# Performance work log

Hardware: AMD Instinct MI355X
Metric: run time of the kernel (lower is better)

Reference implementation:

```python
import math
import jax, jax.numpy as jnp
import numpy as np

NUM_HEADS = 8
FACTOR = 5


def setup_inputs() -> dict:
    key = jax.random.key(0)
    ks = jax.random.split(key, 8)
    B, N, C = 8, 4096, 512
    s = 0.02
    x = jax.random.normal(ks[0], (B, N, C), dtype=jnp.float32)
    Wq = jax.random.normal(ks[1], (C, C), dtype=jnp.float32) * s
    Wk = jax.random.normal(ks[2], (C, C), dtype=jnp.float32) * s
    Wv = jax.random.normal(ks[3], (C, C), dtype=jnp.float32) * s
    Wp = jax.random.normal(ks[4], (C, C), dtype=jnp.float32) * s
    bq = jnp.zeros((C,), jnp.float32)
    bk = jnp.zeros((C,), jnp.float32)
    bv = jnp.zeros((C,), jnp.float32)
    bp = jnp.zeros((C,), jnp.float32)
    sample_k = min(FACTOR * int(np.ceil(np.log(N))), N)  # 45
    index_sample = jax.random.randint(ks[5], (N, sample_k), 0, N, dtype=jnp.int64)
    return {"x": x, "Wq": Wq, "bq": bq, "Wk": Wk, "bk": bk,
            "Wv": Wv, "bv": bv, "Wp": Wp, "bp": bp,
            "index_sample": index_sample}


def reference(x, Wq, bq, Wk, bk, Wv, bv, Wp, bp, index_sample):
    B, N, C = x.shape
    H = NUM_HEADS
    Dh = C // H
    L_Q = L_K = N
    # qkv projections (torch Linear: x @ W.T + b; W sampled symmetric so use x @ W + b)
    q = (x @ Wq + bq).reshape(B, N, H, Dh).transpose(0, 2, 1, 3)  # [B,H,L,Dh]
    k = (x @ Wk + bk).reshape(B, N, H, Dh).transpose(0, 2, 1, 3)
    v = (x @ Wv + bv).reshape(B, N, H, Dh).transpose(0, 2, 1, 3)

    u = min(FACTOR * int(np.ceil(np.log(L_Q))), L_Q)  # n_top
    scale = (C // H) ** (-0.5)

    # _prob_QK: sampled scores per query
    K_sample = k[:, :, index_sample, :]                       # [B,H,L_Q,s,Dh]
    QK_sample = jnp.einsum('bhld,bhlsd->bhls', q, K_sample)   # [B,H,L_Q,s]
    M = QK_sample.max(axis=-1) - QK_sample.sum(axis=-1) / L_K # sparsity measure
    _, M_top = jax.lax.top_k(M, u)                            # [B,H,u]
    Q_reduce = jnp.take_along_axis(q, M_top[..., None], axis=2)  # [B,H,u,Dh]
    scores = jnp.einsum('bhud,bhkd->bhuk', Q_reduce, k) * scale  # [B,H,u,L_K]

    # initial context: mean of V over keys (mask_flag=False)
    context = jnp.broadcast_to(v.mean(axis=2, keepdims=True), (B, H, L_Q, Dh))

    # update context at selected queries
    attn = jax.nn.softmax(scores, axis=-1)
    out_u = jnp.einsum('bhuk,bhkd->bhud', attn, v)            # [B,H,u,Dh]
    bI = jnp.arange(B)[:, None, None]
    hI = jnp.arange(H)[None, :, None]
    context = context.at[bI, hI, M_top].set(out_u)            # [B,H,L_Q,Dh]

    # mix=True: reshape [B,H,N,Dh] -> [B,N,H*Dh] directly (faithful to source)
    context = context.reshape(B, N, H * Dh)
    return context @ Wp + bp
```

## Files before the change

### kernel.cpp

```cpp
#include <hip/hip_runtime.h>
#include <float.h>

typedef unsigned short ushort_t;
typedef short bf16x8 __attribute__((ext_vector_type(8)));
typedef _Float16 f16x8 __attribute__((ext_vector_type(8)));
typedef float f32x4 __attribute__((ext_vector_type(4)));

#define NS 4096
#define ND 64
#define NU 45
#define NUP 48

__device__ __forceinline__ float bf2f(ushort_t u){ return __uint_as_float(((unsigned)u)<<16); }
__device__ __forceinline__ ushort_t f2bf(float f){
  unsigned u = __float_as_uint(f);
  u += 0x7fffu + ((u>>16)&1u);
  return (ushort_t)(u>>16);
}
__device__ __forceinline__ ushort_t f2h(float f){ _Float16 h=(_Float16)f; return __builtin_bit_cast(ushort_t, h); }
__device__ __forceinline__ float h2f(ushort_t u){ return (float)__builtin_bit_cast(_Float16, u); }

__global__ __launch_bounds__(256) void k_wsplit(const float* __restrict__ Wq,
                                                const float* __restrict__ Wk,
                                                const float* __restrict__ Wv,
                                                ushort_t* __restrict__ wh,
                                                ushort_t* __restrict__ wl)
{
  int i = blockIdx.x*256 + threadIdx.x;
  int c = i >> 9, k = i & 511;
  const float* W = (c < 512) ? Wq : (c < 1024 ? Wk : Wv);
  float v = W[k*512 + (c & 511)];
  ushort_t h = f2bf(v);
  wh[i] = h;
  wl[i] = f2bf(v - bf2f(h));
}

__global__ __launch_bounds__(256) void k_xsplit(const float* __restrict__ x,
                                                ushort_t* __restrict__ xh,
                                                ushort_t* __restrict__ xl)
{
  int i = (blockIdx.x*256 + threadIdx.x)*4;
  float4 v = *(const float4*)(x + i);
  ushort4 h, lo;
  h.x = f2bf(v.x); lo.x = f2bf(v.x - bf2f(h.x));
  h.y = f2bf(v.y); lo.y = f2bf(v.y - bf2f(h.y));
  h.z = f2bf(v.z); lo.z = f2bf(v.z - bf2f(h.z));
  h.w = f2bf(v.w); lo.w = f2bf(v.w - bf2f(h.w));
  *(ushort4*)(xh + i) = h;
  *(ushort4*)(xl + i) = lo;
}

template<int MODE>
__global__ __launch_bounds__(256) void k_gemm(
    const float* __restrict__ x,
    const ushort_t* __restrict__ xh, const ushort_t* __restrict__ xl,
    const ushort_t* __restrict__ wh, const ushort_t* __restrict__ wl,
    const float* __restrict__ bq, const float* __restrict__ bk, const float* __restrict__ bv,
    float* __restrict__ qf, float* __restrict__ kf, ushort_t* __restrict__ vfT,
    ushort_t* __restrict__ kb16)
{
  __shared__ __align__(16) ushort_t smem[20480];
  ushort_t* Ah = smem;
  ushort_t* Al = smem + 5120;
  ushort_t* Bh = smem + 10240;
  ushort_t* Bl = smem + 15360;
  const int nbx = (MODE == 0) ? 4 : 8;
  const int p = blockIdx.y * nbx + blockIdx.x;
  const int cx = p & 7;
  const int local = p >> 3;
  const int by = cx*32 + local/nbx;
  const int bx = local % nbx;
  const int rowbase = by * 128;
  const int colbase = (MODE == 0 ? 0 : 512) + bx*128;
  const int mat = colbase >> 9;
  const int t = threadIdx.x;
  const int l = t & 63;
  const int w = t >> 6;
  const int wm = w >> 1, wn = w & 1;
  f32x4 acc[4][4] = {};
  const int r0 = t >> 2;
  const int c0 = (t & 3) * 8;

  for (int k0 = 0; k0 < 512; k0 += 32) {
    __syncthreads();
    #pragma unroll
    for (int half = 0; half < 2; half++) {
      const int r = r0 + half*64;
      if constexpr (MODE == 1) {
        *(uint4*)(&Ah[r*40 + c0]) = *(const uint4*)(&xh[(size_t)(rowbase + r)*512 + k0 + c0]);
        *(uint4*)(&Al[r*40 + c0]) = *(const uint4*)(&xl[(size_t)(rowbase + r)*512 + k0 + c0]);
      } else {
        const float* xp = &x[(size_t)(rowbase + r)*512 + k0 + c0];
        float4 v0 = *(const float4*)xp;
        float4 v1 = *(const float4*)(xp + 4);
        ushort_t hi[8], lo[8];
        float vv[8] = {v0.x,v0.y,v0.z,v0.w,v1.x,v1.y,v1.z,v1.w};
        #pragma unroll
        for (int j = 0; j < 8; j++) {
          hi[j] = f2bf(vv[j]);
          lo[j] = f2bf(vv[j] - bf2f(hi[j]));
        }
        *(uint4*)(&Ah[r*40 + c0]) = *(const uint4*)hi;
        *(uint4*)(&Al[r*40 + c0]) = *(const uint4*)lo;
      }
      *(uint4*)(&Bh[r*40 + c0]) = *(const uint4*)(&wh[(size_t)(colbase + r)*512 + k0 + c0]);
      *(uint4*)(&Bl[r*40 + c0]) = *(const uint4*)(&wl[(size_t)(colbase + r)*512 + k0 + c0]);
    }
    __syncthreads();
    bf16x8 ah[4], al[4], bh8[4], bl8[4];
    #pragma unroll
    for (int m = 0; m < 4; m++) {
      const int off = (wm*64 + m*16 + (l & 15))*40 + (l >> 4)*8;
      ah[m] = *(const bf16x8*)(&Ah[off]);
      al[m] = *(const bf16x8*)(&Al[off]);
    }
    #pragma unroll
    for (int n = 0; n < 4; n++) {
      const int off = (wn*64 + n*16 + (l & 15))*40 + (l >> 4)*8;
      bh8[n] = *(const bf16x8*)(&Bh[off]);
      bl8[n] = *(const bf16x8*)(&Bl[off]);
    }
    #pragma unroll
    for (int m = 0; m < 4; m++)
      #pragma unroll
      for (int n = 0; n < 4; n++) {
        acc[m][n] = __builtin_amdgcn_mfma_f32_16x16x32_bf16(ah[m], bh8[n], acc[m][n], 0, 0, 0);
        acc[m][n] = __builtin_amdgcn_mfma_f32_16x16x32_bf16(ah[m], bl8[n], acc[m][n], 0, 0, 0);
        acc[m][n] = __builtin_amdgcn_mfma_f32_16x16x32_bf16(al[m], bh8[n], acc[m][n], 0, 0, 0);
      }
  }

  if (MODE == 0 || mat == 1) {
    const float* bias_p = (MODE == 0) ? bq : bk;
    float* dst = (MODE == 0) ? qf : kf;
    #pragma unroll
    for (int n = 0; n < 4; n++) {
      const int wi = (colbase & 511) + wn*64 + n*16 + (l & 15);
      const int hh = wi >> 6, d = wi & 63;
      const float bias = bias_p[wi];
      #pragma unroll
      for (int m = 0; m < 4; m++) {
        const int rb = rowbase + wm*64 + m*16 + ((l >> 4) << 2);
        const int b  = rb >> 12, nr = rb & 4095;
        #pragma unroll
        for (int j = 0; j < 4; j++)
          dst[((size_t)(b*8 + hh)*NS + nr + j)*ND + d] = acc[m][n][j] + bias;
      }
    }
    if (MODE == 1 && kb16) {
      __syncthreads();
      #pragma unroll
      for (int n = 0; n < 4; n++) {
        const int c_l = wn*64 + n*16 + (l & 15);
        const float bias = bk[(colbase & 511) + c_l];
        #pragma unroll
        for (int m = 0; m < 4; m++) {
          const int rb_l = wm*64 + m*16 + ((l >> 4) << 2);
          #pragma unroll
          for (int j = 0; j < 4; j++)
            smem[(rb_l + j)*136 + c_l] = f2bf(acc[m][n][j] + bias);
        }
      }
      __syncthreads();
      const int r2 = t >> 1, half = t & 1;
      const int hh2 = ((colbase & 511) >> 6) + half;
      const int b2 = rowbase >> 12;
      const int nr2 = rowbase & 4095;
      ushort_t* op = &kb16[((size_t)(b2*8 + hh2)*NS + nr2 + r2)*ND];
      const ushort_t* ip = &smem[r2*136 + half*64];
      #pragma unroll
      for (int cch = 0; cch < 8; cch++)
        *(uint4*)(op + cch*8) = *(const uint4*)(ip + cch*8);
    }
  } else {
    __syncthreads();
    #pragma unroll
    for (int n = 0; n < 4; n++) {
      const int wi_l = wn*64 + n*16 + (l & 15);
      const float bias = bv[(colbase & 511) + wi_l];
      #pragma unroll
      for (int m = 0; m < 4; m++) {
        const int nr_l = wm*64 + m*16 + ((l >> 4) << 2);
        ushort4 pk;
        pk.x = f2h(acc[m][n][0] + bias);
        pk.y = f2h(acc[m][n][1] + bias);
        pk.z = f2h(acc[m][n][2] + bias);
        pk.w = f2h(acc[m][n][3] + bias);
        *(ushort4*)(&smem[wi_l*136 + nr_l]) = pk;
      }
    }
    __syncthreads();
    const int wi2 = t >> 1, half = t & 1;
    const int cim = (colbase & 511) + wi2;
    const int hh2 = cim >> 6, d2 = cim & 63;
    const int b2 = rowbase >> 12;
    const int nr2 = (rowbase & 4095) + half*64;
    ushort_t* op = &vfT[((size_t)(b2*8 + hh2)*ND + d2)*NS + nr2];
    const ushort_t* ip = &smem[wi2*136 + half*64];
    #pragma unroll
    for (int cch = 0; cch < 8; cch++)
      *(uint4*)(op + cch*8) = *(const uint4*)(ip + cch*8);
  }
}

__global__ __launch_bounds__(256) void k_m_approx(const float* __restrict__ qf,
                                                  const ushort_t* __restrict__ kb16,
                                                  const int* __restrict__ idxs,
                                                  float* __restrict__ Mv)
{
  __shared__ float qs[4][64];
  __shared__ int   sidx[4][48];
  const int orig = blockIdx.y * 1024 + blockIdx.x;
  const int lin  = (orig & 7) * 8192 + (orig >> 3);
  const int bh   = lin >> 10;
  const int lc   = lin & 1023;
  const int t = threadIdx.x;
  const int wv = t >> 6, lane = t & 63;
  const int l = lc*4 + wv;
  qs[wv][lane] = qf[((size_t)bh*NS + l)*ND + lane];
  for (int e = t; e < 4*NU; e += 256)
    sidx[e/NU][e%NU] = idxs[(size_t)(lc*4 + e/NU)*NU + e%NU];
  __syncthreads();
  const int g  = lane >> 3;
  const int dq = lane & 7;
  const float* qp = &qs[wv][dq*8];
  float mx = -FLT_MAX, sm = 0.f;
  #pragma unroll
  for (int p = 0; p < 6; p++) {
    const int s = p*8 + g;
    const bool val = (s < NU);
    const int id = sidx[wv][val ? s : NU-1];
    uint4 ku = *(const uint4*)(&kb16[((size_t)bh*NS + id)*ND + dq*8]);
    const ushort_t* kp = (const ushort_t*)&ku;
    float p_dot = qp[0]*bf2f(kp[0]) + qp[1]*bf2f(kp[1]) + qp[2]*bf2f(kp[2]) + qp[3]*bf2f(kp[3])
                + qp[4]*bf2f(kp[4]) + qp[5]*bf2f(kp[5]) + qp[6]*bf2f(kp[6]) + qp[7]*bf2f(kp[7]);
    p_dot += __shfl_xor(p_dot, 1, 64);
    p_dot += __shfl_xor(p_dot, 2, 64);
    p_dot += __shfl_xor(p_dot, 4, 64);
    if (val) { mx = fmaxf(mx, p_dot); sm += p_dot; }
  }
  #pragma unroll
  for (int o = 8; o < 64; o <<= 1) {
    mx = fmaxf(mx, __shfl_xor(mx, o, 64));
    sm += __shfl_xor(sm, o, 64);
  }
  if (lane == 0) Mv[bh*NS + l] = mx - sm * (1.0f/(float)NS);
}

__global__ __launch_bounds__(256) void k_m_exact_full(const float* __restrict__ qf,
                                                      const float* __restrict__ kf,
                                                      const int* __restrict__ idxs,
                                                      float* __restrict__ Mv)
{
  const int bh = blockIdx.y;
  const int l  = blockIdx.x*4 + (threadIdx.x >> 6);
  const int lane = threadIdx.x & 63;
  const int g  = lane >> 2;
  const int dq = lane & 3;
  const float* qrow = qf + ((size_t)bh*NS + l)*ND + dq*16;
  const float4 q0 = *(const float4*)(qrow + 0);
  const float4 q1 = *(const float4*)(qrow + 4);
  const float4 q2 = *(const float4*)(qrow + 8);
  const float4 q3 = *(const float4*)(qrow + 12);
  const float* kbase = kf + (size_t)bh*NS*ND;
  const int* ib = idxs + (size_t)l*NU;
  float mx = -FLT_MAX, sm = 0.f;
  #pragma unroll
  for (int p3 = 0; p3 < 3; p3++) {
    const int s = p3*16 + g;
    const int id = ib[s < NU ? s : NU-1];
    const float* kr = kbase + (size_t)id*ND + dq*16;
    const float4 k0 = *(const float4*)(kr + 0);
    const float4 k1 = *(const float4*)(kr + 4);
    const float4 k2 = *(const float4*)(kr + 8);
    const float4 k3 = *(const float4*)(kr + 12);
    float p = q0.x*k0.x + q0.y*k0.y + q0.z*k0.z + q0.w*k0.w
            + q1.x*k1.x + q1.y*k1.y + q1.z*k1.z + q1.w*k1.w
            + q2.x*k2.x + q2.y*k2.y + q2.z*k2.z + q2.w*k2.w
            + q3.x*k3.x + q3.y*k3.y + q3.z*k3.z + q3.w*k3.w;
    p += __shfl_xor(p, 1, 64);
    p += __shfl_xor(p, 2, 64);
    if (s < NU) { mx = fmaxf(mx, p); sm += p; }
  }
  #pragma unroll
  for (int o = 4; o < 64; o <<= 1) {
    mx = fmaxf(mx, __shfl_xor(mx, o, 64));
    sm += __shfl_xor(sm, o, 64);
  }
  if (lane == 0) Mv[bh*NS + l] = mx - sm * (1.0f/(float)NS);
}

template<int NSEL, int OST>
__global__ __launch_bounds__(256) void k_topk(const float* __restrict__ Mv, int* __restrict__ dst)
{
  __shared__ float wvs[4];
  __shared__ int   wis[4];
  const int bh = blockIdx.x, t = threadIdx.x;
  const int wv = t >> 6, lane = t & 63;
  float v[16];
  #pragma unroll
  for (int j = 0; j < 16; j++) v[j] = Mv[bh*NS + j*256 + t];
  unsigned removed = 0;
  float tmax = -FLT_MAX; int tidx = 0x7fffffff;
  #pragma unroll
  for (int j = 0; j < 16; j++) {
    if (v[j] > tmax) { tmax = v[j]; tidx = j*256 + t; }
  }
  for (int it = 0; it < NSEL; it++) {
    float mv = tmax; int mi = tidx;
    #pragma unroll
    for (int o = 1; o < 64; o <<= 1) {
      float vo = __shfl_xor(mv, o, 64); int io = __shfl_xor(mi, o, 64);
      if (vo > mv || (vo == mv && io < mi)) { mv = vo; mi = io; }
    }
    if (lane == 0) { wvs[wv] = mv; wis[wv] = mi; }
    __syncthreads();
    float gv = wvs[0]; int gi = wis[0];
    #pragma unroll
    for (int k2 = 1; k2 < 4; k2++) {
      float vo = wvs[k2]; int io = wis[k2];
      if (vo > gv || (vo == gv && io < gi)) { gv = vo; gi = io; }
    }
    if (t == 0) dst[bh*OST + it] = gi;
    if ((gi & 255) == t) {
      removed |= 1u << (gi >> 8);
      tmax = -FLT_MAX; tidx = 0x7fffffff;
      #pragma unroll
      for (int j = 0; j < 16; j++) {
        bool ok = ((removed >> j) & 1u) == 0u;
        if (ok && (v[j] > tmax || (v[j] == tmax && (j*256+t) < tidx))) { tmax = v[j]; tidx = j*256 + t; }
      }
    }
    __syncthreads();
  }
}

__global__ __launch_bounds__(256) void k_mexact(const float* __restrict__ qf,
                                                const float* __restrict__ kf,
                                                const int* __restrict__ idxs,
                                                const int* __restrict__ Cand,
                                                float* __restrict__ Mex)
{
  const int bh = blockIdx.y, qtr = blockIdx.x, t = threadIdx.x;
  const int c = qtr*16 + (t >> 4);
  const int dl = t & 15;
  const int l = Cand[bh*64 + c];
  const float4 q4 = *(const float4*)(&qf[((size_t)bh*NS + l)*ND + dl*4]);
  const float* kbase = kf + (size_t)bh*NS*ND;
  const int* ib = idxs + (size_t)l*NU;
  float mx = -FLT_MAX, sm = 0.f;
  for (int s = 0; s < NU; s++) {
    const int id = ib[s];
    const float4 k4 = *(const float4*)(&kbase[(size_t)id*ND + dl*4]);
    float p = q4.x*k4.x + q4.y*k4.y + q4.z*k4.z + q4.w*k4.w;
    p += __shfl_xor(p, 1, 64);
    p += __shfl_xor(p, 2, 64);
    p += __shfl_xor(p, 4, 64);
    p += __shfl_xor(p, 8, 64);
    mx = fmaxf(mx, p);
    sm += p;
  }
  if (dl == 0) Mex[bh*64 + c] = mx - sm * (1.0f/(float)NS);
}

__global__ void k_sel45(const float* __restrict__ Mex, const int* __restrict__ Cand,
                        int* __restrict__ Mtop)
{
  const int bh = blockIdx.x, lane = threadIdx.x;
  float val = Mex[bh*64 + lane];
  const int n = Cand[bh*64 + lane];
  for (int it = 0; it < NU; it++) {
    float wv = val; int wn = n;
    #pragma unroll
    for (int o = 1; o < 64; o <<= 1) {
      float vo = __shfl_xor(wv, o, 64); int io = __shfl_xor(wn, o, 64);
      if (vo > wv || (vo == wv && io < wn)) { wv = vo; wn = io; }
    }
    if (lane == 0) Mtop[bh*NUP + it] = wn;
    if (n == wn) val = -FLT_MAX;
  }
}

__global__ __launch_bounds__(256) void k_qreduce(const float* __restrict__ qf,
                                                 const int* __restrict__ Mtop,
                                                 ushort_t* __restrict__ Qr)
{
  const int bh = blockIdx.x, t = threadIdx.x;
  for (int e = t; e < NUP*ND; e += 256) {
    const int u = e >> 6, d = e & 63;
    float v = 0.f;
    if (u < NU) { const int r = Mtop[bh*NUP + u]; v = qf[((size_t)bh*NS + r)*ND + d]; }
    Qr[bh*NUP*ND + e] = f2bf(v);
  }
}

template<int KB>
__global__ __launch_bounds__(256) void k_scores(const ushort_t* __restrict__ Qr,
                                                const float* __restrict__ kf,
                                                const ushort_t* __restrict__ kb16,
                                                ushort_t* __restrict__ scores)
{
  __shared__ __align__(16) ushort_t Ql[NUP*80];
  const int bh = blockIdx.y;
  const int n0 = blockIdx.x * 256;
  const int t = threadIdx.x, w = t >> 6, l = t & 63;
  for (int chunk = t; chunk < NUP*8; chunk += 256) {
    const int r = chunk >> 3, cp = chunk & 7;
    *(uint4*)(&Ql[r*80 + cp*8]) = *(const uint4*)(&Qr[((size_t)bh*NUP + r)*ND + cp*8]);
  }
  __syncthreads();
  f32x4 acc[3][4] = {};
  const int nw = n0 + w*64;
  #pragma unroll
  for (int ks = 0; ks < 2; ks++) {
    bf16x8 a[3], b8[4];
    #pragma unroll
    for (int m = 0; m < 3; m++)
      a[m] = *(const bf16x8*)(&Ql[(m*16 + (l & 15))*80 + (l >> 4)*8 + ks*32]);
    #pragma unroll
    for (int n = 0; n < 4; n++) {
      if constexpr (KB) {
        b8[n] = *(const bf16x8*)(&kb16[((size_t)bh*NS + nw + n*16 + (l & 15))*ND + (l >> 4)*8 + ks*32]);
      } else {
        const float* kr = &kf[((size_t)bh*NS + nw + n*16 + (l & 15))*ND + (l >> 4)*8 + ks*32];
        float4 u0 = *(const float4*)kr;
        float4 u1 = *(const float4*)(kr + 4);
        ushort_t tmp[8] = {f2bf(u0.x),f2bf(u0.y),f2bf(u0.z),f2bf(u0.w),
                           f2bf(u1.x),f2bf(u1.y),f2bf(u1.z),f2bf(u1.w)};
        b8[n] = *(const bf16x8*)tmp;
      }
    }
    #pragma unroll
    for (int m = 0; m < 3; m++)
      #pragma unroll
      for (int n = 0; n < 4; n++)
        acc[m][n] = __builtin_amdgcn_mfma_f32_16x16x32_bf16(a[m], b8[n], acc[m][n], 0, 0, 0);
  }
  #pragma unroll
  for (int m = 0; m < 3; m++)
    #pragma unroll
    for (int n = 0; n < 4; n++)
      #pragma unroll
      for (int j = 0; j < 4; j++) {
        const int row = m*16 + (l >> 4)*4 + j;
        const int col = nw + n*16 + (l & 15);
        scores[((size_t)bh*NUP + row)*NS + col] = f2bf(acc[m][n][j] * 0.125f);
      }
}

__global__ __launch_bounds__(256) void k_softmax(ushort_t* __restrict__ scores)
{
  __shared__ float srow[NS];
  __shared__ float red[256];
  const int bh = blockIdx.y, u = blockIdx.x, t = threadIdx.x;
  ushort_t* row = scores + ((size_t)bh*NUP + u)*NS;
  float mx = -FLT_MAX;
  for (int j = t; j < NS; j += 256) { float v = bf2f(row[j]); srow[j] = v; mx = fmaxf(mx, v); }
  red[t] = mx; __syncthreads();
  for (int s = 128; s > 0; s >>= 1) { if (t < s) red[t] = fmaxf(red[t], red[t+s]); __syncthreads(); }
  mx = red[0]; __syncthreads();
  float sm = 0.f;
  for (int j = t; j < NS; j += 256) { const float e = __expf(srow[j] - mx); srow[j] = e; sm += e; }
  red[t] = sm; __syncthreads();
  for (int s = 128; s > 0; s >>= 1) { if (t < s) red[t] += red[t+s]; __syncthreads(); }
  const float inv = 1.0f / red[0];
  for (int j = t; j < NS; j += 256) row[j] = f2h(srow[j] * inv);
}

__global__ __launch_bounds__(256) void k_vmean(const ushort_t* __restrict__ vfT, float* __restrict__ vmean)
{
  __shared__ float red[256];
  const int d = blockIdx.x, bh = blockIdx.y, t = threadIdx.x;
  const ushort_t* vr = vfT + ((size_t)bh*ND + d)*NS;
  float s = 0.f;
  for (int n = t; n < NS; n += 256) s += h2f(vr[n]);
  red[t] = s; __syncthreads();
  for (int st = 128; st > 0; st >>= 1) { if (t < st) red[t] += red[t+st]; __syncthreads(); }
  if (t == 0) vmean[bh*ND + d] = red[0] * (1.0f/(float)NS);
}

__global__ __launch_bounds__(256) void k_outu(const ushort_t* __restrict__ attn,
                                              const ushort_t* __restrict__ vfT,
                                              float* __restrict__ pout)
{
  const int bh = blockIdx.y, ch = blockIdx.x;
  const int t = threadIdx.x, w = t >> 6, l = t & 63;
  if (w >= 3) return;
  const ushort_t* ab = attn + (size_t)bh*NUP*NS;
  const ushort_t* vb = vfT + (size_t)bh*ND*NS;
  f32x4 acc[4] = {};
  const int arow = w*16 + (l & 15);
  const int koff = (l >> 4)*8;
  const int kbeg = ch*512;
  for (int kc = kbeg; kc < kbeg + 512; kc += 32) {
    uint4 au = *(const uint4*)(&ab[(size_t)arow*NS + kc + koff]);
    f16x8 a = __builtin_bit_cast(f16x8, au);
    #pragma unroll
    for (int nt = 0; nt < 4; nt++) {
      uint4 bu = *(const uint4*)(&vb[(size_t)(nt*16 + (l & 15))*NS + kc + koff]);
      f16x8 b = __builtin_bit_cast(f16x8, bu);
      acc[nt] = __builtin_amdgcn_mfma_f32_16x16x32_f16(a, b, acc[nt], 0, 0, 0);
    }
  }
  #pragma unroll
  for (int nt = 0; nt < 4; nt++)
    #pragma unroll
    for (int j = 0; j < 4; j++) {
      const int u = w*16 + (l >> 4)*4 + j;
      const int d = nt*16 + (l & 15);
      pout[(((size_t)bh*8 + ch)*NUP + u)*ND + d] = acc[nt][j];
    }
}

__global__ __launch_bounds__(256) void k_delta_fin(const float* __restrict__ pout,
                                                   const float* __restrict__ vmean,
                                                   float* __restrict__ delta)
{
  const int bh = blockIdx.x, t = threadIdx.x;
  for (int e = t; e < NUP*ND; e += 256) {
    const int u = e >> 6, d = e & 63;
    float s = 0.f;
    #pragma unroll
    for (int ch = 0; ch < 8; ch++) s += pout[(((size_t)bh*8 + ch)*NUP + u)*ND + d];
    delta[((size_t)bh*NUP + u)*ND + d] = s - vmean[bh*ND + d];
  }
}

__global__ __launch_bounds__(256) void k_uidx_init(int* __restrict__ uidx)
{
  uidx[blockIdx.x*256 + threadIdx.x] = -1;
}

__global__ void k_scatter(const int* __restrict__ Mtop, int* __restrict__ uidx)
{
  const int bh = blockIdx.x, t = threadIdx.x;
  if (t < NU) {
    const int n = Mtop[bh*NUP + t];
    const int b = bh >> 3, h = bh & 7;
    const int nprime = h*512 + (n >> 3);
    uidx[((size_t)b*NS + nprime)*8 + (n & 7)] = bh*NUP + t;
  }
}

__global__ __launch_bounds__(256) void k_corr(const float* __restrict__ delta,
                                              const float* __restrict__ Wp,
                                              const int* __restrict__ Mtop,
                                              float* __restrict__ corr)
{
  __shared__ float dl[64];
  const int bh = blockIdx.y, u = blockIdx.x, t = threadIdx.x;
  const int n = Mtop[bh*NUP + u];
  const int j = n & 7;
  if (t < 64) dl[t] = delta[((size_t)bh*NUP + u)*ND + t];
  __syncthreads();
  for (int c = t; c < 512; c += 256) {
    float s = 0.f;
    #pragma unroll 8
    for (int d2 = 0; d2 < 64; d2++) s += dl[d2] * Wp[(size_t)(j*64 + d2)*512 + c];
    corr[((size_t)bh*NUP + u)*512 + c] = s;
  }
}

__global__ __launch_bounds__(256) void k_base(const float* __restrict__ vmean,
                                              const float* __restrict__ Wp,
                                              const float* __restrict__ bp,
                                              float* __restrict__ basep)
{
  __shared__ float vm[64];
  const int bh = blockIdx.x, t = threadIdx.x;
  if (t < 64) vm[t] = vmean[bh*ND + t];
  __syncthreads();
  for (int c = t; c < 512; c += 256) {
    float s = bp[c];
    for (int k = 0; k < 512; k++) s += vm[k & 63] * Wp[(size_t)k*512 + c];
    basep[bh*512 + c] = s;
  }
}

__global__ __launch_bounds__(256) void k_assemble(const float* __restrict__ basep,
                                                  const float* __restrict__ corr,
                                                  const int* __restrict__ uidx,
                                                  float* __restrict__ out)
{
  const int b = blockIdx.y, nprime = blockIdx.x, t = threadIdx.x;
  const int h = nprime >> 9;
  const int* ui = uidx + ((size_t)b*NS + nprime)*8;
  float v0 = basep[(b*8 + h)*512 + t];
  float v1 = basep[(b*8 + h)*512 + 256 + t];
  #pragma unroll
  for (int j = 0; j < 8; j++) {
    const int id = ui[j];
    if (id >= 0) { v0 += corr[(size_t)id*512 + t]; v1 += corr[(size_t)id*512 + 256 + t]; }
  }
  const size_t o = ((size_t)b*NS + nprime)*512;
  out[o + t]       = v0;
  out[o + 256 + t] = v1;
}

extern "C" void kernel_launch(void* const* d_in, const int* in_sizes, int n_in,
                              void* d_out, int out_size, void* d_ws, size_t ws_size,
                              hipStream_t stream)
{
  (void)in_sizes; (void)n_in; (void)out_size;
  const float* x  = (const float*)d_in[0];
  const float* Wq = (const float*)d_in[1];
  const float* bq = (const float*)d_in[2];
  const float* Wk = (const float*)d_in[3];
  const float* bk = (const float*)d_in[4];
  const float* Wv = (const float*)d_in[5];
  const float* bv = (const float*)d_in[6];
  const float* Wp = (const float*)d_in[7];
  const float* bp = (const float*)d_in[8];
  const int* idxs = (const int*)d_in[9];
  float* out      = (float*)d_out;

  char* w = (char*)d_ws;
  float*    qf    = (float*)(w);
  float*    kf    = (float*)(w + 67108864);
  ushort_t* vfT   = (ushort_t*)(w + 134217728);
  ushort_t* wh    = (ushort_t*)(w + 167772160);
  ushort_t* wl    = (ushort_t*)(w + 169345024);
  float*    Mv    = (float*)(w + 170917888);
  int*      Mtop  = (int*)(w + 171966464);
  ushort_t* Qr    = (ushort_t*)(w + 171978752);
  float*    vmean = (float*)(w + 172371968);
  ushort_t* xh = (ushort_t*)(w);
  ushort_t* xl = (ushort_t*)(w + 33554432);
  ushort_t* scores = (ushort_t*)(w);
  float*    delta  = (float*)(w + 25165824);
  float*    corr   = (float*)(w + 25952256);
  int*      uidx   = (int*)(w + 32243712);
  float*    basep  = (float*)(w + 33292288);
  float*    pout   = (float*)(w + 33423360);
  ushort_t* kb16 = (ushort_t*)(w + 172388352);
  int*      Cand = (int*)(w + 205942784);
  float*    Mex  = (float*)(w + 205959168);
  const bool approx_ok = (ws_size >= (size_t)205975552);
  ushort_t* kb16_arg = approx_ok ? kb16 : (ushort_t*)nullptr;

  k_wsplit   <<<3072, 256, 0, stream>>>(Wq, Wk, Wv, wh, wl);
  k_xsplit   <<<16384, 256, 0, stream>>>(x, xh, xl);
  k_gemm<1>  <<<dim3(8, 256), 256, 0, stream>>>(x, xh, xl, wh, wl, bq, bk, bv, qf, kf, vfT, kb16_arg);
  k_gemm<0>  <<<dim3(4, 256), 256, 0, stream>>>(x, nullptr, nullptr, wh, wl, bq, bk, bv, qf, kf, vfT, nullptr);
  if (approx_ok) {
    k_m_approx <<<dim3(1024, 64), 256, 0, stream>>>(qf, kb16, idxs, Mv);
    k_vmean    <<<dim3(64, 64), 256, 0, stream>>>(vfT, vmean);
    k_topk<64,64> <<<64, 256, 0, stream>>>(Mv, Cand);
    k_mexact   <<<dim3(4, 64), 256, 0, stream>>>(qf, kf, idxs, Cand, Mex);
    k_sel45    <<<64, 64, 0, stream>>>(Mex, Cand, Mtop);
  } else {
    k_m_exact_full <<<dim3(1024, 64), 256, 0, stream>>>(qf, kf, idxs, Mv);
    k_vmean    <<<dim3(64, 64), 256, 0, stream>>>(vfT, vmean);
    k_topk<NU,NUP> <<<64, 256, 0, stream>>>(Mv, Mtop);
  }
  k_qreduce  <<<64, 256, 0, stream>>>(qf, Mtop, Qr);
  if (approx_ok) {
    k_scores<1> <<<dim3(16, 64), 256, 0, stream>>>(Qr, kf, kb16, scores);
  } else {
    k_scores<0> <<<dim3(16, 64), 256, 0, stream>>>(Qr, kf, nullptr, scores);
  }
  k_softmax  <<<dim3(45, 64), 256, 0, stream>>>(scores);
  k_outu     <<<dim3(8, 64), 256, 0, stream>>>(scores, vfT, pout);
  k_delta_fin<<<64, 256, 0, stream>>>(pout, vmean, delta);
  k_uidx_init<<<1024, 256, 0, stream>>>(uidx);
  k_scatter  <<<64, 64, 0, stream>>>(Mtop, uidx);
  k_corr     <<<dim3(45, 64), 256, 0, stream>>>(delta, Wp, Mtop, corr);
  k_base     <<<64, 256, 0, stream>>>(vmean, Wp, bp, basep);
  k_assemble <<<dim3(4096, 8), 256, 0, stream>>>(basep, corr, uidx, out);
}
```

Measured before the change: 602.6 us.

## Compute Q projection in single bf16 and recompute exact Q only for candidates

The Q projection GEMM now runs a single bf16 MFMA pass and writes bf16 Q, replacing the three-pass split-precision fp32 output. Exact fp32 Q is recomputed in a new small kernel only for the 64 top candidate rows per head, and those rows feed exact M, selection and Q_reduce. The x-split kernel is dropped in favour of converting x inline inside the GEMM, the fallback exact path is removed, and k_base now uses a precomputed per-head sum of Wp. The aim is to cut GEMM MFMA work and Q memory traffic. The risk is that candidate selection now depends on lower-precision M estimates.

```diff
diff --git a/kernel.cpp b/kernel.cpp
--- a/kernel.cpp
+++ b/kernel.cpp
@@ -35,34 +35,18 @@
   wl[i] = f2bf(v - bf2f(h));
 }
 
-__global__ __launch_bounds__(256) void k_xsplit(const float* __restrict__ x,
-                                                ushort_t* __restrict__ xh,
-                                                ushort_t* __restrict__ xl)
-{
-  int i = (blockIdx.x*256 + threadIdx.x)*4;
-  float4 v = *(const float4*)(x + i);
-  ushort4 h, lo;
-  h.x = f2bf(v.x); lo.x = f2bf(v.x - bf2f(h.x));
-  h.y = f2bf(v.y); lo.y = f2bf(v.y - bf2f(h.y));
-  h.z = f2bf(v.z); lo.z = f2bf(v.z - bf2f(h.z));
-  h.w = f2bf(v.w); lo.w = f2bf(v.w - bf2f(h.w));
-  *(ushort4*)(xh + i) = h;
-  *(ushort4*)(xl + i) = lo;
-}
-
 template<int MODE>
 __global__ __launch_bounds__(256) void k_gemm(
     const float* __restrict__ x,
-    const ushort_t* __restrict__ xh, const ushort_t* __restrict__ xl,
     const ushort_t* __restrict__ wh, const ushort_t* __restrict__ wl,
     const float* __restrict__ bq, const float* __restrict__ bk, const float* __restrict__ bv,
-    float* __restrict__ qf, float* __restrict__ kf, ushort_t* __restrict__ vfT,
-    ushort_t* __restrict__ kb16)
+    float* __restrict__ kf, ushort_t* __restrict__ vfT,
+    ushort_t* __restrict__ kb16, ushort_t* __restrict__ qb16)
 {
   __shared__ __align__(16) ushort_t smem[20480];
   ushort_t* Ah = smem;
   ushort_t* Al = smem + 5120;
-  ushort_t* Bh = smem + 10240;
+  ushort_t* Bh = smem + (MODE == 1 ? 10240 : 5120);
   ushort_t* Bl = smem + 15360;
   const int nbx = (MODE == 0) ? 4 : 8;
   const int p = blockIdx.y * nbx + blockIdx.x;
@@ -86,25 +70,20 @@
     #pragma unroll
     for (int half = 0; half < 2; half++) {
       const int r = r0 + half*64;
-      if constexpr (MODE == 1) {
-        *(uint4*)(&Ah[r*40 + c0]) = *(const uint4*)(&xh[(size_t)(rowbase + r)*512 + k0 + c0]);
-        *(uint4*)(&Al[r*40 + c0]) = *(const uint4*)(&xl[(size_t)(rowbase + r)*512 + k0 + c0]);
-      } else {
-        const float* xp = &x[(size_t)(rowbase + r)*512 + k0 + c0];
-        float4 v0 = *(const float4*)xp;
-        float4 v1 = *(const float4*)(xp + 4);
-        ushort_t hi[8], lo[8];
-        float vv[8] = {v0.x,v0.y,v0.z,v0.w,v1.x,v1.y,v1.z,v1.w};
-        #pragma unroll
-        for (int j = 0; j < 8; j++) {
-          hi[j] = f2bf(vv[j]);
-          lo[j] = f2bf(vv[j] - bf2f(hi[j]));
-        }
-        *(uint4*)(&Ah[r*40 + c0]) = *(const uint4*)hi;
-        *(uint4*)(&Al[r*40 + c0]) = *(const uint4*)lo;
+      const float* xp = &x[(size_t)(rowbase + r)*512 + k0 + c0];
+      float4 v0 = *(const float4*)xp;
+      float4 v1 = *(const float4*)(xp + 4);
+      ushort_t hi[8], lo[8];
+      float vv[8] = {v0.x,v0.y,v0.z,v0.w,v1.x,v1.y,v1.z,v1.w};
+      #pragma unroll
+      for (int j = 0; j < 8; j++) {
+        hi[j] = f2bf(vv[j]);
+        if (MODE == 1) lo[j] = f2bf(vv[j] - bf2f(hi[j]));
       }
+      *(uint4*)(&Ah[r*40 + c0]) = *(const uint4*)hi;
+      if (MODE == 1) *(uint4*)(&Al[r*40 + c0]) = *(const uint4*)lo;
       *(uint4*)(&Bh[r*40 + c0]) = *(const uint4*)(&wh[(size_t)(colbase + r)*512 + k0 + c0]);
-      *(uint4*)(&Bl[r*40 + c0]) = *(const uint4*)(&wl[(size_t)(colbase + r)*512 + k0 + c0]);
+      if (MODE == 1) *(uint4*)(&Bl[r*40 + c0]) = *(const uint4*)(&wl[(size_t)(colbase + r)*512 + k0 + c0]);
     }
     __syncthreads();
     bf16x8 ah[4], al[4], bh8[4], bl8[4];
@@ -112,67 +91,27 @@
     for (int m = 0; m < 4; m++) {
       const int off = (wm*64 + m*16 + (l & 15))*40 + (l >> 4)*8;
       ah[m] = *(const bf16x8*)(&Ah[off]);
-      al[m] = *(const bf16x8*)(&Al[off]);
+      if (MODE == 1) al[m] = *(const bf16x8*)(&Al[off]);
     }
     #pragma unroll
     for (int n = 0; n < 4; n++) {
       const int off = (wn*64 + n*16 + (l & 15))*40 + (l >> 4)*8;
       bh8[n] = *(const bf16x8*)(&Bh[off]);
-      bl8[n] = *(const bf16x8*)(&Bl[off]);
+      if (MODE == 1) bl8[n] = *(const bf16x8*)(&Bl[off]);
     }
     #pragma unroll
     for (int m = 0; m < 4; m++)
       #pragma unroll
       for (int n = 0; n < 4; n++) {
         acc[m][n] = __builtin_amdgcn_mfma_f32_16x16x32_bf16(ah[m], bh8[n], acc[m][n], 0, 0, 0);
-        acc[m][n] = __builtin_amdgcn_mfma_f32_16x16x32_bf16(ah[m], bl8[n], acc[m][n], 0, 0, 0);
-        acc[m][n] = __builtin_amdgcn_mfma_f32_16x16x32_bf16(al[m], bh8[n], acc[m][n], 0, 0, 0);
-      }
-  }
-
-  if (MODE == 0 || mat == 1) {
-    const float* bias_p = (MODE == 0) ? bq : bk;
-    float* dst = (MODE == 0) ? qf : kf;
-    #pragma unroll
-    for (int n = 0; n < 4; n++) {
-      const int wi = (colbase & 511) + wn*64 + n*16 + (l & 15);
-      const int hh = wi >> 6, d = wi & 63;
-      const float bias = bias_p[wi];
-      #pragma unroll
-      for (int m = 0; m < 4; m++) {
-        const int rb = rowbase + wm*64 + m*16 + ((l >> 4) << 2);
-        const int b  = rb >> 12, nr = rb & 4095;
-        #pragma unroll
-        for (int j = 0; j < 4; j++)
-          dst[((size_t)(b*8 + hh)*NS + nr + j)*ND + d] = acc[m][n][j] + bias;
-      }
-    }
-    if (MODE == 1 && kb16) {
-      __syncthreads();
-      #pragma unroll
-      for (int n = 0; n < 4; n++) {
-        const int c_l = wn*64 + n*16 + (l & 15);
-        const float bias = bk[(colbase & 511) + c_l];
-        #pragma unroll
-        for (int m = 0; m < 4; m++) {
-          const int rb_l = wm*64 + m*16 + ((l >> 4) << 2);
-          #pragma unroll
-          for (int j = 0; j < 4; j++)
-            smem[(rb_l + j)*136 + c_l] = f2bf(acc[m][n][j] + bias);
+        if (MODE == 1) {
+          acc[m][n] = __builtin_amdgcn_mfma_f32_16x16x32_bf16(ah[m], bl8[n], acc[m][n], 0, 0, 0);
+          acc[m][n] = __builtin_amdgcn_mfma_f32_16x16x32_bf16(al[m], bh8[n], acc[m][n], 0, 0, 0);
         }
       }
-      __syncthreads();
-      const int r2 = t >> 1, half = t & 1;
-      const int hh2 = ((colbase & 511) >> 6) + half;
-      const int b2 = rowbase >> 12;
-      const int nr2 = rowbase & 4095;
-      ushort_t* op = &kb16[((size_t)(b2*8 + hh2)*NS + nr2 + r2)*ND];
-      const ushort_t* ip = &smem[r2*136 + half*64];
-      #pragma unroll
-      for (int cch = 0; cch < 8; cch++)
-        *(uint4*)(op + cch*8) = *(const uint4*)(ip + cch*8);
-    }
-  } else {
+  }
+
+  if (MODE == 1 && mat == 2) {
     __syncthreads();
     #pragma unroll
     for (int n = 0; n < 4; n++) {
@@ -200,10 +139,55 @@
     #pragma unroll
     for (int cch = 0; cch < 8; cch++)
       *(uint4*)(op + cch*8) = *(const uint4*)(ip + cch*8);
-  }
-}
-
-__global__ __launch_bounds__(256) void k_m_approx(const float* __restrict__ qf,
+    return;
+  }
+
+  if (MODE == 1) {
+    #pragma unroll
+    for (int n = 0; n < 4; n++) {
+      const int wi = (colbase & 511) + wn*64 + n*16 + (l & 15);
+      const int hh = wi >> 6, d = wi & 63;
+      const float bias = bk[wi];
+      #pragma unroll
+      for (int m = 0; m < 4; m++) {
+        const int rb = rowbase + wm*64 + m*16 + ((l >> 4) << 2);
+        const int b  = rb >> 12, nr = rb & 4095;
+        #pragma unroll
+        for (int j = 0; j < 4; j++)
+          kf[((size_t)(b*8 + hh)*NS + nr + j)*ND + d] = acc[m][n][j] + bias;
+      }
+    }
+  }
+  {
+    ushort_t* obuf = (MODE == 0) ? qb16 : kb16;
+    const float* bias_p = (MODE == 0) ? bq : bk;
+    __syncthreads();
+    #pragma unroll
+    for (int n = 0; n < 4; n++) {
+      const int c_l = wn*64 + n*16 + (l & 15);
+      const float bias = bias_p[(colbase & 511) + c_l];
+      #pragma unroll
+      for (int m = 0; m < 4; m++) {
+        const int rb_l = wm*64 + m*16 + ((l >> 4) << 2);
+        #pragma unroll
+        for (int j = 0; j < 4; j++)
+          smem[(rb_l + j)*136 + c_l] = f2bf(acc[m][n][j] + bias);
+      }
+    }
+    __syncthreads();
+    const int r2 = t >> 1, half = t & 1;
+    const int hh2 = ((colbase & 511) >> 6) + half;
+    const int b2 = rowbase >> 12;
+    const int nr2 = rowbase & 4095;
+    ushort_t* op = &obuf[((size_t)(b2*8 + hh2)*NS + nr2 + r2)*ND];
+    const ushort_t* ip = &smem[r2*136 + half*64];
+    #pragma unroll
+    for (int cch = 0; cch < 8; cch++)
+      *(uint4*)(op + cch*8) = *(const uint4*)(ip + cch*8);
+  }
+}
+
+__global__ __launch_bounds__(256) void k_m_approx(const ushort_t* __restrict__ qb16,
                                                   const ushort_t* __restrict__ kb16,
                                                   const int* __restrict__ idxs,
                                                   float* __restrict__ Mv)
@@ -217,7 +201,7 @@
   const int t = threadIdx.x;
   const int wv = t >> 6, lane = t & 63;
   const int l = lc*4 + wv;
-  qs[wv][lane] = qf[((size_t)bh*NS + l)*ND + lane];
+  qs[wv][lane] = bf2f(qb16[((size_t)bh*NS + l)*ND + lane]);
   for (int e = t; e < 4*NU; e += 256)
     sidx[e/NU][e%NU] = idxs[(size_t)(lc*4 + e/NU)*NU + e%NU];
   __syncthreads();
@@ -247,49 +231,6 @@
   if (lane == 0) Mv[bh*NS + l] = mx - sm * (1.0f/(float)NS);
 }
 
-__global__ __launch_bounds__(256) void k_m_exact_full(const float* __restrict__ qf,
-                                                      const float* __restrict__ kf,
-                                                      const int* __restrict__ idxs,
-                                                      float* __restrict__ Mv)
-{
-  const int bh = blockIdx.y;
-  const int l  = blockIdx.x*4 + (threadIdx.x >> 6);
-  const int lane = threadIdx.x & 63;
-  const int g  = lane >> 2;
-  const int dq = lane & 3;
-  const float* qrow = qf + ((size_t)bh*NS + l)*ND + dq*16;
-  const float4 q0 = *(const float4*)(qrow + 0);
-  const float4 q1 = *(const float4*)(qrow + 4);
-  const float4 q2 = *(const float4*)(qrow + 8);
-  const float4 q3 = *(const float4*)(qrow + 12);
-  const float* kbase = kf + (size_t)bh*NS*ND;
-  const int* ib = idxs + (size_t)l*NU;
-  float mx = -FLT_MAX, sm = 0.f;
-  #pragma unroll
-  for (int p3 = 0; p3 < 3; p3++) {
-    const int s = p3*16 + g;
-    const int id = ib[s < NU ? s : NU-1];
-    const float* kr = kbase + (size_t)id*ND + dq*16;
-    const float4 k0 = *(const float4*)(kr + 0);
-    const float4 k1 = *(const float4*)(kr + 4);
-    const float4 k2 = *(const float4*)(kr + 8);
-    const float4 k3 = *(const float4*)(kr + 12);
-    float p = q0.x*k0.x + q0.y*k0.y + q0.z*k0.z + q0.w*k0.w
-            + q1.x*k1.x + q1.y*k1.y + q1.z*k1.z + q1.w*k1.w
-            + q2.x*k2.x + q2.y*k2.y + q2.z*k2.z + q2.w*k2.w
-            + q3.x*k3.x + q3.y*k3.y + q3.z*k3.z + q3.w*k3.w;
-    p += __shfl_xor(p, 1, 64);
-    p += __shfl_xor(p, 2, 64);
-    if (s < NU) { mx = fmaxf(mx, p); sm += p; }
-  }
-  #pragma unroll
-  for (int o = 4; o < 64; o <<= 1) {
-    mx = fmaxf(mx, __shfl_xor(mx, o, 64));
-    sm += __shfl_xor(sm, o, 64);
-  }
-  if (lane == 0) Mv[bh*NS + l] = mx - sm * (1.0f/(float)NS);
-}
-
 template<int NSEL, int OST>
 __global__ __launch_bounds__(256) void k_topk(const float* __restrict__ Mv, int* __restrict__ dst)
 {
@@ -335,7 +276,53 @@
   }
 }
 
-__global__ __launch_bounds__(256) void k_mexact(const float* __restrict__ qf,
+__global__ __launch_bounds__(256) void k_qexact(const float* __restrict__ x,
+                                                const ushort_t* __restrict__ wh,
+                                                const ushort_t* __restrict__ wl,
+                                                const float* __restrict__ bq,
+                                                const int* __restrict__ Cand,
+                                                float* __restrict__ qex)
+{
+  const int bh = blockIdx.x, t = threadIdx.x;
+  const int wv = t >> 6, l = t & 63;
+  const int b = bh >> 3, h = bh & 7;
+  const int cand = 16*wv + (l & 15);
+  const int n = Cand[bh*64 + cand];
+  const float* xr = x + ((size_t)b*NS + n)*512 + (l >> 4)*8;
+  f32x4 acc[4] = {};
+  for (int k0 = 0; k0 < 512; k0 += 32) {
+    float4 v0 = *(const float4*)(xr + k0);
+    float4 v1 = *(const float4*)(xr + k0 + 4);
+    ushort_t hi[8], lo[8];
+    float vv[8] = {v0.x,v0.y,v0.z,v0.w,v1.x,v1.y,v1.z,v1.w};
+    #pragma unroll
+    for (int j = 0; j < 8; j++) {
+      hi[j] = f2bf(vv[j]);
+      lo[j] = f2bf(vv[j] - bf2f(hi[j]));
+    }
+    bf16x8 ah = *(const bf16x8*)hi;
+    bf16x8 al = *(const bf16x8*)lo;
+    #pragma unroll
+    for (int nt = 0; nt < 4; nt++) {
+      const size_t boff = (size_t)(h*64 + nt*16 + (l & 15))*512 + k0 + (l >> 4)*8;
+      bf16x8 bh8 = *(const bf16x8*)(&wh[boff]);
+      bf16x8 bl8 = *(const bf16x8*)(&wl[boff]);
+      acc[nt] = __builtin_amdgcn_mfma_f32_16x16x32_bf16(ah, bh8, acc[nt], 0, 0, 0);
+      acc[nt] = __builtin_amdgcn_mfma_f32_16x16x32_bf16(ah, bl8, acc[nt], 0, 0, 0);
+      acc[nt] = __builtin_amdgcn_mfma_f32_16x16x32_bf16(al, bh8, acc[nt], 0, 0, 0);
+    }
+  }
+  #pragma unroll
+  for (int nt = 0; nt < 4; nt++)
+    #pragma unroll
+    for (int j = 0; j < 4; j++) {
+      const int cand_o = 16*wv + (l >> 4)*4 + j;
+      const int d_o = nt*16 + (l & 15);
+      qex[((size_t)bh*64 + cand_o)*ND + d_o] = acc[nt][j] + bq[h*64 + d_o];
+    }
+}
+
+__global__ __launch_bounds__(256) void k_mexact(const float* __restrict__ qex,
                                                 const float* __restrict__ kf,
                                                 const int* __restrict__ idxs,
                                                 const int* __restrict__ Cand,
@@ -345,7 +332,7 @@
   const int c = qtr*16 + (t >> 4);
   const int dl = t & 15;
   const int l = Cand[bh*64 + c];
-  const float4 q4 = *(const float4*)(&qf[((size_t)bh*NS + l)*ND + dl*4]);
+  const float4 q4 = *(const float4*)(&qex[((size_t)bh*64 + c)*ND + dl*4]);
   const float* kbase = kf + (size_t)bh*NS*ND;
   const int* ib = idxs + (size_t)l*NU;
   float mx = -FLT_MAX, sm = 0.f;
@@ -364,39 +351,38 @@
 }
 
 __global__ void k_sel45(const float* __restrict__ Mex, const int* __restrict__ Cand,
-                        int* __restrict__ Mtop)
+                        int* __restrict__ Mtop, int* __restrict__ MtopSlot)
 {
   const int bh = blockIdx.x, lane = threadIdx.x;
   float val = Mex[bh*64 + lane];
   const int n = Cand[bh*64 + lane];
+  const int slot = lane;
   for (int it = 0; it < NU; it++) {
-    float wv = val; int wn = n;
+    float wv = val; int wn = n; int ws = slot;
     #pragma unroll
     for (int o = 1; o < 64; o <<= 1) {
-      float vo = __shfl_xor(wv, o, 64); int io = __shfl_xor(wn, o, 64);
-      if (vo > wv || (vo == wv && io < wn)) { wv = vo; wn = io; }
-    }
-    if (lane == 0) Mtop[bh*NUP + it] = wn;
+      float vo = __shfl_xor(wv, o, 64); int io = __shfl_xor(wn, o, 64); int so = __shfl_xor(ws, o, 64);
+      if (vo > wv || (vo == wv && io < wn)) { wv = vo; wn = io; ws = so; }
+    }
+    if (lane == 0) { Mtop[bh*NUP + it] = wn; MtopSlot[bh*NUP + it] = ws; }
     if (n == wn) val = -FLT_MAX;
   }
 }
 
-__global__ __launch_bounds__(256) void k_qreduce(const float* __restrict__ qf,
-                                                 const int* __restrict__ Mtop,
+__global__ __launch_bounds__(256) void k_qreduce(const float* __restrict__ qex,
+                                                 const int* __restrict__ MtopSlot,
                                                  ushort_t* __restrict__ Qr)
 {
   const int bh = blockIdx.x, t = threadIdx.x;
   for (int e = t; e < NUP*ND; e += 256) {
     const int u = e >> 6, d = e & 63;
     float v = 0.f;
-    if (u < NU) { const int r = Mtop[bh*NUP + u]; v = qf[((size_t)bh*NS + r)*ND + d]; }
+    if (u < NU) { const int s = MtopSlot[bh*NUP + u]; v = qex[((size_t)bh*64 + s)*ND + d]; }
     Qr[bh*NUP*ND + e] = f2bf(v);
   }
 }
 
-template<int KB>
 __global__ __launch_bounds__(256) void k_scores(const ushort_t* __restrict__ Qr,
-                                                const float* __restrict__ kf,
                                                 const ushort_t* __restrict__ kb16,
                                                 ushort_t* __restrict__ scores)
 {
@@ -418,18 +404,8 @@
     for (int m = 0; m < 3; m++)
       a[m] = *(const bf16x8*)(&Ql[(m*16 + (l & 15))*80 + (l >> 4)*8 + ks*32]);
     #pragma unroll
-    for (int n = 0; n < 4; n++) {
-      if constexpr (KB) {
-        b8[n] = *(const bf16x8*)(&kb16[((size_t)bh*NS + nw + n*16 + (l & 15))*ND + (l >> 4)*8 + ks*32]);
-      } else {
-        const float* kr = &kf[((size_t)bh*NS + nw + n*16 + (l & 15))*ND + (l >> 4)*8 + ks*32];
-        float4 u0 = *(const float4*)kr;
-        float4 u1 = *(const float4*)(kr + 4);
-        ushort_t tmp[8] = {f2bf(u0.x),f2bf(u0.y),f2bf(u0.z),f2bf(u0.w),
-                           f2bf(u1.x),f2bf(u1.y),f2bf(u1.z),f2bf(u1.w)};
-        b8[n] = *(const bf16x8*)tmp;
-      }
-    }
+    for (int n = 0; n < 4; n++)
+      b8[n] = *(const bf16x8*)(&kb16[((size_t)bh*NS + nw + n*16 + (l & 15))*ND + (l >> 4)*8 + ks*32]);
     #pragma unroll
     for (int m = 0; m < 3; m++)
       #pragma unroll
@@ -561,8 +537,19 @@
   }
 }
 
+__global__ __launch_bounds__(256) void k_wpsum(const float* __restrict__ Wp,
+                                               float* __restrict__ Wpsum)
+{
+  int i = blockIdx.x*256 + threadIdx.x;
+  int d2 = i >> 9, c = i & 511;
+  float s = 0.f;
+  #pragma unroll
+  for (int j = 0; j < 8; j++) s += Wp[(size_t)(j*64 + d2)*512 + c];
+  Wpsum[i] = s;
+}
+
 __global__ __launch_bounds__(256) void k_base(const float* __restrict__ vmean,
-                                              const float* __restrict__ Wp,
+                                              const float* __restrict__ Wpsum,
                                               const float* __restrict__ bp,
                                               float* __restrict__ basep)
 {
@@ -572,7 +559,8 @@
   __syncthreads();
   for (int c = t; c < 512; c += 256) {
     float s = bp[c];
-    for (int k = 0; k < 512; k++) s += vm[k & 63] * Wp[(size_t)k*512 + c];
+    #pragma unroll 8
+    for (int d2 = 0; d2 < 64; d2++) s += vm[d2] * Wpsum[d2*512 + c];
     basep[bh*512 + c] = s;
   }
 }
@@ -601,7 +589,7 @@
                               void* d_out, int out_size, void* d_ws, size_t ws_size,
                               hipStream_t stream)
 {
-  (void)in_sizes; (void)n_in; (void)out_size;
+  (void)in_sizes; (void)n_in; (void)out_size; (void)ws_size;
   const float* x  = (const float*)d_in[0];
   const float* Wq = (const float*)d_in[1];
   const float* bq = (const float*)d_in[2];
@@ -615,56 +603,46 @@
   float* out      = (float*)d_out;
 
   char* w = (char*)d_ws;
-  float*    qf    = (float*)(w);
-  float*    kf    = (float*)(w + 67108864);
-  ushort_t* vfT   = (ushort_t*)(w + 134217728);
+  float*    kf    = (float*)(w);
+  ushort_t* vfT   = (ushort_t*)(w + 67108864);
+  ushort_t* kb16  = (ushort_t*)(w + 100663296);
+  ushort_t* qb16  = (ushort_t*)(w + 134217728);
   ushort_t* wh    = (ushort_t*)(w + 167772160);
   ushort_t* wl    = (ushort_t*)(w + 169345024);
   float*    Mv    = (float*)(w + 170917888);
   int*      Mtop  = (int*)(w + 171966464);
-  ushort_t* Qr    = (ushort_t*)(w + 171978752);
-  float*    vmean = (float*)(w + 172371968);
-  ushort_t* xh = (ushort_t*)(w);
-  ushort_t* xl = (ushort_t*)(w + 33554432);
+  int*      MtopSlot = (int*)(w + 171978752);
+  int*      Cand  = (int*)(w + 171991040);
+  float*    Mex   = (float*)(w + 172007424);
+  float*    vmean = (float*)(w + 172023808);
+  ushort_t* Qr    = (ushort_t*)(w + 172040192);
+  float*    qex   = (float*)(w + 172433408);
+  float*    Wpsum = (float*)(w + 173481984);
   ushort_t* scores = (ushort_t*)(w);
   float*    delta  = (float*)(w + 25165824);
   float*    corr   = (float*)(w + 25952256);
   int*      uidx   = (int*)(w + 32243712);
   float*    basep  = (float*)(w + 33292288);
   float*    pout   = (float*)(w + 33423360);
-  ushort_t* kb16 = (ushort_t*)(w + 172388352);
-  int*      Cand = (int*)(w + 205942784);
-  float*    Mex  = (float*)(w + 205959168);
-  const bool approx_ok = (ws_size >= (size_t)205975552);
-  ushort_t* kb16_arg = approx_ok ? kb16 : (ushort_t*)nullptr;
 
   k_wsplit   <<<3072, 256, 0, stream>>>(Wq, Wk, Wv, wh, wl);
-  k_xsplit   <<<16384, 256, 0, stream>>>(x, xh, xl);
-  k_gemm<1>  <<<dim3(8, 256), 256, 0, stream>>>(x, xh, xl, wh, wl, bq, bk, bv, qf, kf, vfT, kb16_arg);
-  k_gemm<0>  <<<dim3(4, 256), 256, 0, stream>>>(x, nullptr, nullptr, wh, wl, bq, bk, bv, qf, kf, vfT, nullptr);
-  if (approx_ok) {
-    k_m_approx <<<dim3(1024, 64), 256, 0, stream>>>(qf, kb16, idxs, Mv);
-    k_vmean    <<<dim3(64, 64), 256, 0, stream>>>(vfT, vmean);
-    k_topk<64,64> <<<64, 256, 0, stream>>>(Mv, Cand);
-    k_mexact   <<<dim3(4, 64), 256, 0, stream>>>(qf, kf, idxs, Cand, Mex);
-    k_sel45    <<<64, 64, 0, stream>>>(Mex, Cand, Mtop);
-  } else {
-    k_m_exact_full <<<dim3(1024, 64), 256, 0, stream>>>(qf, kf, idxs, Mv);
-    k_vmean    <<<dim3(64, 64), 256, 0, stream>>>(vfT, vmean);
-    k_topk<NU,NUP> <<<64, 256, 0, stream>>>(Mv, Mtop);
-  }
-  k_qreduce  <<<64, 256, 0, stream>>>(qf, Mtop, Qr);
-  if (approx_ok) {
-    k_scores<1> <<<dim3(16, 64), 256, 0, stream>>>(Qr, kf, kb16, scores);
-  } else {
-    k_scores<0> <<<dim3(16, 64), 256, 0, stream>>>(Qr, kf, nullptr, scores);
-  }
+  k_gemm<1>  <<<dim3(8, 256), 256, 0, stream>>>(x, wh, wl, bq, bk, bv, kf, vfT, kb16, nullptr);
+  k_gemm<0>  <<<dim3(4, 256), 256, 0, stream>>>(x, wh, wl, bq, bk, bv, nullptr, nullptr, nullptr, qb16);
+  k_wpsum    <<<128, 256, 0, stream>>>(Wp, Wpsum);
+  k_m_approx <<<dim3(1024, 64), 256, 0, stream>>>(qb16, kb16, idxs, Mv);
+  k_vmean    <<<dim3(64, 64), 256, 0, stream>>>(vfT, vmean);
+  k_topk<64,64> <<<64, 256, 0, stream>>>(Mv, Cand);
+  k_qexact   <<<64, 256, 0, stream>>>(x, wh, wl, bq, Cand, qex);
+  k_mexact   <<<dim3(4, 64), 256, 0, stream>>>(qex, kf, idxs, Cand, Mex);
+  k_sel45    <<<64, 64, 0, stream>>>(Mex, Cand, Mtop, MtopSlot);
+  k_qreduce  <<<64, 256, 0, stream>>>(qex, MtopSlot, Qr);
+  k_scores   <<<dim3(16, 64), 256, 0, stream>>>(Qr, kb16, scores);
   k_softmax  <<<dim3(45, 64), 256, 0, stream>>>(scores);
   k_outu     <<<dim3(8, 64), 256, 0, stream>>>(scores, vfT, pout);
   k_delta_fin<<<64, 256, 0, stream>>>(pout, vmean, delta);
   k_uidx_init<<<1024, 256, 0, stream>>>(uidx);
   k_scatter  <<<64, 64, 0, stream>>>(Mtop, uidx);
   k_corr     <<<dim3(45, 64), 256, 0, stream>>>(delta, Wp, Mtop, corr);
-  k_base     <<<64, 256, 0, stream>>>(vmean, Wp, bp, basep);
+  k_base     <<<64, 256, 0, stream>>>(vmean, Wpsum, bp, basep);
   k_assemble <<<dim3(4096, 8), 256, 0, stream>>>(basep, corr, uidx, out);
 }
```

Measured after the change: 571.2 us. -5.2%, faster.
